# Performance work log

Hardware: AMD Instinct MI355X
Metric: run time of the kernel (lower is better)

The kernel has to match this reference:

```python
import jax, jax.numpy as jnp
import numpy as np

B, S, H, T, W = 8, 512, 768, 4, 10
NEG = -1e9

def _u(key, shape, k):
    return jax.random.uniform(key, shape, jnp.float32, -k, k)

def setup_inputs():
    key = jax.random.key(0)
    ks = jax.random.split(key, 20)
    kh = float(1.0 / np.sqrt(H)); kt = float(1.0 / np.sqrt(T))
    return dict(
        embeddings=jax.random.normal(ks[0], (B, S, H), jnp.float32),
        l1f_wih=_u(ks[1], (4 * H, H), kh), l1f_whh=_u(ks[2], (4 * H, H), kh), l1f_b=_u(ks[3], (4 * H,), kh),
        l1r_wih=_u(ks[4], (4 * H, H), kh), l1r_whh=_u(ks[5], (4 * H, H), kh), l1r_b=_u(ks[6], (4 * H,), kh),
        attn_w=_u(ks[7], (3 * H,), kh), attn_b=_u(ks[8], (1,), kh),
        l2f_wih=_u(ks[9], (4 * T, 2 * H), kt), l2f_whh=_u(ks[10], (4 * T, T), kt), l2f_b=_u(ks[11], (4 * T,), kt),
        l2r_wih=_u(ks[12], (4 * T, 2 * H), kt), l2r_whh=_u(ks[13], (4 * T, T), kt), l2r_b=_u(ks[14], (4 * T,), kt),
        crf_start=0.1 * jax.random.normal(ks[15], (T,), jnp.float32),
        crf_end=0.1 * jax.random.normal(ks[16], (T,), jnp.float32),
        crf_trans=0.1 * jax.random.normal(ks[17], (T, T), jnp.float32),
        window_size=W,
    )

def _lstm_dir(x, w_ih, w_hh, b):
    # x: [B,S,D] -> [B,S,Hh]; torch gate order i,f,g,o
    Hh = w_hh.shape[1]
    bs = x.shape[0]
    xs = (jnp.einsum('bsd,gd->bsg', x, w_ih) + b).transpose(1, 0, 2)  # [S,B,4Hh]
    def step(carry, xt):
        h, c = carry
        g = xt + h @ w_hh.T
        i, f, gg, o = jnp.split(g, 4, axis=-1)
        c = jax.nn.sigmoid(f) * c + jax.nn.sigmoid(i) * jnp.tanh(gg)
        h = jax.nn.sigmoid(o) * jnp.tanh(c)
        return (h, c), h
    init = (jnp.zeros((bs, Hh), x.dtype), jnp.zeros((bs, Hh), x.dtype))
    _, hs = jax.lax.scan(step, init, xs)
    return hs.transpose(1, 0, 2)

def _bilstm(x, pf, pr):
    hf = _lstm_dir(x, *pf)
    hr = _lstm_dir(x[:, ::-1], *pr)[:, ::-1]
    return jnp.concatenate([hf, hr], axis=-1)

def _win_attn(h, w, b, win):
    # h: [B,S,D]; similarity(hi,hj) = w1.hi + w2.hj + w3.(hi*hj) + b
    bs, s, d = h.shape
    w1, w2, w3 = w[:d], w[d:2 * d], w[2 * d:]
    offs = jnp.arange(-win, win + 1)                      # [K]
    idx = jnp.arange(s)[:, None] + offs[None, :]          # [S,K]
    valid = (idx >= 0) & (idx < s)
    idxc = jnp.clip(idx, 0, s - 1)
    hw = h[:, idxc]                                       # [B,S,K,D]
    scores = (h @ w1)[:, :, None] \
        + jnp.einsum('bskd,d->bsk', hw, w2) \
        + jnp.einsum('bsd,bskd->bsk', h * w3, hw) + b[0]
    scores = jnp.where(valid[None], scores, NEG)
    aw = jax.nn.softmax(scores, axis=-1)                  # [B,S,K]
    return jnp.einsum('bsk,bskd->bsd', aw, hw)

def _viterbi(em, start, end, trans):
    # em: [B,S,T] -> tags [B,S]
    score0 = start[None] + em[:, 0]
    ems = em.transpose(1, 0, 2)[1:]                       # [S-1,B,T]
    def step(score, e_t):
        nxt = score[:, :, None] + trans[None]             # [B,Tprev,T]
        best = jnp.max(nxt, axis=1) + e_t
        bp = jnp.argmax(nxt, axis=1)
        return best, bp
    final, bps = jax.lax.scan(step, score0, ems)          # bps [S-1,B,T]
    final = final + end[None]
    last = jnp.argmax(final, axis=-1)                     # [B]
    def back(tag, bp):
        prev = jnp.take_along_axis(bp, tag[:, None], axis=1)[:, 0]
        return prev, prev
    _, tags_rev = jax.lax.scan(back, last, bps[::-1])
    return jnp.concatenate([tags_rev[::-1], last[None]], axis=0).transpose(1, 0)

def reference(embeddings, l1f_wih, l1f_whh, l1f_b, l1r_wih, l1r_whh, l1r_b,
              attn_w, attn_b, l2f_wih, l2f_whh, l2f_b, l2r_wih, l2r_whh, l2r_b,
              crf_start, crf_end, crf_trans, window_size):
    h1 = _bilstm(embeddings, (l1f_wih, l1f_whh, l1f_b), (l1r_wih, l1r_whh, l1r_b))
    d = h1.shape[-1] // 2
    hs = h1[..., :d] + h1[..., d:]                        # sum of directions [B,S,H]
    att = _win_attn(hs, attn_w, attn_b, int(window_size))
    x2 = jnp.concatenate([hs, att], axis=-1)              # [B,S,2H]
    h2 = _bilstm(x2, (l2f_wih, l2f_whh, l2f_b), (l2r_wih, l2r_whh, l2r_b))
    d2 = h2.shape[-1] // 2
    em = h2[..., :d2] + h2[..., d2:]                      # CRF emissions [B,S,T]
    tags = _viterbi(em, crf_start, crf_end, crf_trans)
    return tags, em
```

## Files before the change

### kernel.cpp

```cpp
#include <hip/hip_runtime.h>
#include <math.h>

#define SEQ 512
#define BATCH 8
#define HID 768
#define G4 3072
#define CHUNK 128
#define NEGV (-1000000000.0f)

typedef float v4f __attribute__((ext_vector_type(4)));

__device__ __forceinline__ float sigm(float x) { return 1.0f / (1.0f + expf(-x)); }

__device__ __forceinline__ float wred(float x) {
#pragma unroll
  for (int off = 32; off > 0; off >>= 1) x += __shfl_xor(x, off, 64);
  return x;
}

__device__ __forceinline__ void load2_f4_sc(const float* p0, const float* p1,
                                            v4f& a, v4f& b) {
  asm volatile("global_load_dwordx4 %0, %2, off sc0 sc1\n\t"
               "global_load_dwordx4 %1, %3, off sc0 sc1\n\t"
               "s_waitcnt vmcnt(0)"
               : "=&v"(a), "=&v"(b) : "v"(p0), "v"(p1) : "memory");
}
__device__ __forceinline__ int load_i_sc(const int* p) {
  int r;
  asm volatile("global_load_dword %0, %1, off sc0 sc1\n\ts_waitcnt vmcnt(0)"
               : "=v"(r) : "v"(p) : "memory");
  return r;
}
__device__ __forceinline__ void store_f_sc(float* p, float v) {
  asm volatile("global_store_dword %0, %1, off sc0 sc1" :: "v"(p), "v"(v) : "memory");
}
__device__ __forceinline__ void store_i_sc(int* p, int v) {
  asm volatile("global_store_dword %0, %1, off sc0 sc1" :: "v"(p), "v"(v) : "memory");
}

template <int CTRL, int RMASK>
__device__ __forceinline__ float dpp_add(float x) {
  int y = __builtin_amdgcn_update_dpp(0, __float_as_int(x), CTRL, RMASK, 0xF, false);
  return x + __int_as_float(y);
}
__device__ __forceinline__ float reduce32(float x) {
  x = dpp_add<0x121, 0xF>(x);
  x = dpp_add<0x122, 0xF>(x);
  x = dpp_add<0x124, 0xF>(x);
  x = dpp_add<0x128, 0xF>(x);
  x = dpp_add<0x142, 0xA>(x);
  return x;
}

__global__ void k_init(float* __restrict__ hbuf, int* __restrict__ flags) {
  int i = blockIdx.x * blockDim.x + threadIdx.x;
  if (i < 2 * 2 * BATCH * HID) hbuf[i] = 0.0f;
  if (i < 4096) flags[i] = 0;
}

__global__ __launch_bounds__(256) void k_proj1(
    const float* __restrict__ emb,
    const float* __restrict__ w_f, const float* __restrict__ b_f,
    const float* __restrict__ w_r, const float* __restrict__ b_r,
    float* __restrict__ xs_f, float* __restrict__ xs_r, int chunk) {
  __shared__ float As[16][132];
  __shared__ float Bs[16][132];
  const int tid = threadIdx.x;
  const int bn0 = blockIdx.x * 128;
  const int bb  = blockIdx.y;
  const int dir = blockIdx.z;
  const float* W    = dir ? w_r : w_f;
  const float* bias = dir ? b_r : b_f;
  float* xs = dir ? xs_r : xs_f;

  float acc[8][8];
#pragma unroll
  for (int i = 0; i < 8; i++)
#pragma unroll
    for (int j = 0; j < 8; j++) acc[i][j] = 0.0f;

  const int mload = tid & 127;
  const int kq0   = tid >> 7;
  const int tglob = dir ? (SEQ - 1 - (chunk * CHUNK + mload)) : (chunk * CHUNK + mload);
  const float* arow = emb + (size_t)(bb * SEQ + tglob) * HID;
  const float* brow = W + (size_t)(bn0 + mload) * HID;
  const int tm = tid & 15, tn = tid >> 4;

  for (int kt = 0; kt < HID; kt += 16) {
#pragma unroll
    for (int rep = 0; rep < 2; rep++) {
      int kq = kq0 + rep * 2;
      float4 a = *(const float4*)(arow + kt + kq * 4);
      As[kq * 4 + 0][mload] = a.x; As[kq * 4 + 1][mload] = a.y;
      As[kq * 4 + 2][mload] = a.z; As[kq * 4 + 3][mload] = a.w;
      float4 b = *(const float4*)(brow + kt + kq * 4);
      Bs[kq * 4 + 0][mload] = b.x; Bs[kq * 4 + 1][mload] = b.y;
      Bs[kq * 4 + 2][mload] = b.z; Bs[kq * 4 + 3][mload] = b.w;
    }
    __syncthreads();
#pragma unroll
    for (int k = 0; k < 16; k++) {
      float4 a0 = *(const float4*)&As[k][tm * 8];
      float4 a1 = *(const float4*)&As[k][tm * 8 + 4];
      float4 b0 = *(const float4*)&Bs[k][tn * 8];
      float4 b1 = *(const float4*)&Bs[k][tn * 8 + 4];
      float av[8] = {a0.x, a0.y, a0.z, a0.w, a1.x, a1.y, a1.z, a1.w};
      float bv[8] = {b0.x, b0.y, b0.z, b0.w, b1.x, b1.y, b1.z, b1.w};
#pragma unroll
      for (int i = 0; i < 8; i++)
#pragma unroll
        for (int j = 0; j < 8; j++) acc[i][j] += av[i] * bv[j];
    }
    __syncthreads();
  }
#pragma unroll
  for (int i = 0; i < 8; i++) {
    int row = tm * 8 + i;
    size_t base = (size_t)(bb * CHUNK + row) * G4 + bn0 + tn * 8;
#pragma unroll
    for (int j = 0; j < 8; j++) xs[base + j] = acc[i][j] + bias[bn0 + tn * 8 + j];
  }
}

__global__ __launch_bounds__(384, 2) void k_rec1(
    const float* __restrict__ whh_f, const float* __restrict__ whh_r,
    const float* __restrict__ xs_f, const float* __restrict__ xs_r,
    float* __restrict__ hbuf, float* __restrict__ cbuf, int* __restrict__ flags,
    float* __restrict__ hf, float* __restrict__ hr, int t0, int init) {
  __shared__ float hlds[4 * HID];
  const int tid = threadIdx.x;
  const int bid = blockIdx.x;
  const int dir = bid >> 7;
  const int bh  = (bid >> 6) & 1;
  const int jb  = bid & 63;
  const int J0  = jb * 12;
  const int grp = dir * 2 + bh;
  const int g  = tid >> 5;
  const int kq = tid & 31;
  const int j  = J0 + g;

  const float* W  = dir ? whh_r : whh_f;
  const float* xs = dir ? xs_r  : xs_f;
  float* harr = dir ? hr : hf;

  float wreg[4][24];
#pragma unroll
  for (int gate = 0; gate < 4; gate++) {
#pragma unroll
    for (int q = 0; q < 6; q++) {
      *(v4f*)&wreg[gate][q * 4] =
          *(const v4f*)&W[(size_t)(gate * HID + j) * HID + q * 128 + kq * 4];
    }
  }

  float cc[4];
#pragma unroll
  for (int b = 0; b < 4; b++) cc[b] = 0.0f;
  if (!init && kq == 16) {
#pragma unroll
    for (int b = 0; b < 4; b++) cc[b] = cbuf[bid * 48 + g * 4 + b];
  }

  for (int stp = 0; stp < CHUNK; stp++) {
    const int s = t0 + stp;
    const int par = s & 1;

    float xsv[4][4];
    if (kq == 16) {
#pragma unroll
      for (int b = 0; b < 4; b++) {
        const size_t xbase = (size_t)((bh * 4 + b) * CHUNK + stp) * G4 + j;
#pragma unroll
        for (int gate = 0; gate < 4; gate++)
          xsv[b][gate] = xs[xbase + gate * HID];
      }
    }

    if (tid < 64) {
      const int* fp = flags + (grp * 64 + tid) * 16;
      while (load_i_sc(fp) < s) { __builtin_amdgcn_s_sleep(4); }
    }
    __syncthreads();

    {
      const float* src = hbuf + (size_t)((par * 2 + dir) * BATCH + bh * 4) * HID + tid * 8;
      v4f a, b4;
      load2_f4_sc(src, src + 4, a, b4);
      *(v4f*)&hlds[tid * 8]     = a;
      *(v4f*)&hlds[tid * 8 + 4] = b4;
    }
    __syncthreads();

    float acc[4][4];
#pragma unroll
    for (int gate = 0; gate < 4; gate++)
#pragma unroll
      for (int b = 0; b < 4; b++) acc[gate][b] = 0.0f;
#pragma unroll
    for (int b = 0; b < 4; b++) {
      float hk[24];
#pragma unroll
      for (int q = 0; q < 6; q++)
        *(v4f*)&hk[q * 4] = *(const v4f*)&hlds[b * HID + q * 128 + kq * 4];
#pragma unroll
      for (int gate = 0; gate < 4; gate++)
#pragma unroll
        for (int k = 0; k < 24; k++) acc[gate][b] += wreg[gate][k] * hk[k];
    }
#pragma unroll
    for (int gate = 0; gate < 4; gate++)
#pragma unroll
      for (int b = 0; b < 4; b++) acc[gate][b] = reduce32(acc[gate][b]);

    if (kq == 16) {
      const int t = dir ? (SEQ - 1 - s) : s;
#pragma unroll
      for (int b = 0; b < 4; b++) {
        const int bg = bh * 4 + b;
        float iv = acc[0][b] + xsv[b][0];
        float fv = acc[1][b] + xsv[b][1];
        float gv = acc[2][b] + xsv[b][2];
        float ov = acc[3][b] + xsv[b][3];
        cc[b] = sigm(fv) * cc[b] + sigm(iv) * tanhf(gv);
        float h = sigm(ov) * tanhf(cc[b]);
        store_f_sc(hbuf + (size_t)(((par ^ 1) * 2 + dir) * BATCH + bg) * HID + j, h);
        harr[(size_t)(bg * SEQ + t) * HID + j] = h;
      }
    }
    asm volatile("s_waitcnt vmcnt(0)" ::: "memory");
    __syncthreads();
    if (tid == 0) store_i_sc(flags + (grp * 64 + jb) * 16, s + 1);
  }
  if (kq == 16) {
#pragma unroll
    for (int b = 0; b < 4; b++) cbuf[bid * 48 + g * 4 + b] = cc[b];
  }
}

__global__ void k_sum(float* __restrict__ hf, const float* __restrict__ hr) {
  int i = blockIdx.x * 256 + threadIdx.x;
  float4 a = ((const float4*)hf)[i];
  float4 b = ((const float4*)hr)[i];
  a.x += b.x; a.y += b.y; a.z += b.z; a.w += b.w;
  ((float4*)hf)[i] = a;
}

__global__ __launch_bounds__(64) void k_attn(
    const float* __restrict__ hs, const float* __restrict__ attn_w,
    const float* __restrict__ attn_b, float* __restrict__ att) {
  const int l = threadIdx.x;
  const int s = blockIdx.x, b = blockIdx.y;
  const float* hrow = hs + (size_t)(b * SEQ + s) * HID;
  float v[12];
  float u1p = 0.0f;
#pragma unroll
  for (int jj = 0; jj < 12; jj++) {
    int d = l + 64 * jj;
    float x = hrow[d];
    u1p += x * attn_w[d];
    v[jj] = attn_w[HID + d] + x * attn_w[2 * HID + d];
  }
  float u1 = wred(u1p) + attn_b[0];
  float sc[21];
  for (int o = 0; o < 21; o++) {
    int s2 = s + o - 10;
    if (s2 >= 0 && s2 < SEQ) {
      const float* h2 = hs + (size_t)(b * SEQ + s2) * HID;
      float p = 0.0f;
#pragma unroll
      for (int jj = 0; jj < 12; jj++) p += h2[l + 64 * jj] * v[jj];
      sc[o] = wred(p) + u1;
    } else {
      sc[o] = NEGV;
    }
  }
  float m = sc[0];
#pragma unroll
  for (int o = 1; o < 21; o++) m = fmaxf(m, sc[o]);
  float sum = 0.0f;
#pragma unroll
  for (int o = 0; o < 21; o++) { sc[o] = expf(sc[o] - m); sum += sc[o]; }
  float inv = 1.0f / sum;
  float acc[12];
#pragma unroll
  for (int jj = 0; jj < 12; jj++) acc[jj] = 0.0f;
  for (int o = 0; o < 21; o++) {
    int s2 = s + o - 10;
    if (s2 < 0 || s2 >= SEQ) continue;
    float a = sc[o] * inv;
    const float* h2 = hs + (size_t)(b * SEQ + s2) * HID;
#pragma unroll
    for (int jj = 0; jj < 12; jj++) acc[jj] += a * h2[l + 64 * jj];
  }
  float* orow = att + (size_t)(b * SEQ + s) * HID;
#pragma unroll
  for (int jj = 0; jj < 12; jj++) orow[l + 64 * jj] = acc[jj];
}

__global__ __launch_bounds__(256) void k_proj2(
    const float* __restrict__ hs, const float* __restrict__ att,
    const float* __restrict__ w2f, const float* __restrict__ b2f,
    const float* __restrict__ w2r, const float* __restrict__ b2r,
    float* __restrict__ xs2) {
  __shared__ __align__(16) float x2[2 * HID];
  __shared__ float part[32][9];
  const int tid = threadIdx.x;
  const int s = blockIdx.x, b = blockIdx.y;
  size_t base = (size_t)(b * SEQ + s) * HID;
  for (int i = tid; i < 2 * HID; i += 256)
    x2[i] = (i < HID) ? hs[base + i] : att[base + i - HID];
  __syncthreads();
  const int gid = tid & 31, pp = tid >> 5;
  const int d = gid >> 4, g = gid & 15;
  const float4* w4 = (const float4*)((d ? w2r : w2f) + (size_t)g * (2 * HID));
  const float4* x4 = (const float4*)x2;
  float p = 0.0f;
  for (int e = pp * 48; e < pp * 48 + 48; e++) {
    float4 xv = x4[e];
    float4 wv = w4[e];
    p += xv.x * wv.x + xv.y * wv.y + xv.z * wv.z + xv.w * wv.w;
  }
  part[gid][pp] = p;
  __syncthreads();
  if (tid < 32) {
    float sumv = (d ? b2r : b2f)[g];
#pragma unroll
    for (int q = 0; q < 8; q++) sumv += part[gid][q];
    xs2[(size_t)((d * BATCH + b) * SEQ + s) * 16 + g] = sumv;
  }
}

__global__ __launch_bounds__(256) void k_rec2(
    const float* __restrict__ xs2,
    const float* __restrict__ whh_f, const float* __restrict__ whh_r,
    float* __restrict__ h2) {
  __shared__ float hsh[2 * BATCH * 4];
  __shared__ float gsh[2 * BATCH * 16];
  const int tid = threadIdx.x;
  const int d = tid >> 7, b = (tid >> 4) & 7, g = tid & 15;
  const float* whh = (d ? whh_r : whh_f) + g * 4;
  const float w0 = whh[0], w1 = whh[1], w2 = whh[2], w3 = whh[3];
  const int hb = d * BATCH + b;
  if (g < 4) hsh[hb * 4 + g] = 0.0f;
  float c = 0.0f;
  __syncthreads();
  const float* xrow = xs2 + (size_t)hb * SEQ * 16 + g;
  for (int st = 0; st < SEQ; st++) {
    int t = d ? (SEQ - 1 - st) : st;
    float gv = xrow[t * 16] + w0 * hsh[hb * 4 + 0] + w1 * hsh[hb * 4 + 1] +
               w2 * hsh[hb * 4 + 2] + w3 * hsh[hb * 4 + 3];
    gsh[hb * 16 + g] = gv;
    __syncthreads();
    if (g < 4) {
      float iv = gsh[hb * 16 + g];
      float fv = gsh[hb * 16 + 4 + g];
      float gq = gsh[hb * 16 + 8 + g];
      float ov = gsh[hb * 16 + 12 + g];
      c = sigm(fv) * c + sigm(iv) * tanhf(gq);
      float h = sigm(ov) * tanhf(c);
      hsh[hb * 4 + g] = h;
      h2[((size_t)hb * SEQ + t) * 4 + g] = h;
    }
    __syncthreads();
  }
}

__global__ void k_em(const float* __restrict__ h2, float* __restrict__ out) {
  int i = blockIdx.x * 256 + threadIdx.x;
  if (i < BATCH * SEQ * 4) out[BATCH * SEQ + i] = h2[i] + h2[BATCH * SEQ * 4 + i];
}

__global__ __launch_bounds__(32) void k_viterbi(
    float* __restrict__ out, const float* __restrict__ start,
    const float* __restrict__ endw, const float* __restrict__ trans) {
  __shared__ unsigned char bp[SEQ - 1][32];
  const int l = threadIdx.x;
  const int b = l >> 2, j = l & 3;
  const float* em = out + BATCH * SEQ;
  const float tr0 = trans[0 * 4 + j], tr1 = trans[1 * 4 + j];
  const float tr2 = trans[2 * 4 + j], tr3 = trans[3 * 4 + j];
  float score = start[j] + em[((size_t)b * SEQ + 0) * 4 + j];
  for (int t = 1; t < SEQ; t++) {
    float s0 = __shfl(score, b * 4 + 0, 64);
    float s1 = __shfl(score, b * 4 + 1, 64);
    float s2 = __shfl(score, b * 4 + 2, 64);
    float s3 = __shfl(score, b * 4 + 3, 64);
    float v0 = s0 + tr0, v1 = s1 + tr1, v2 = s2 + tr2, v3 = s3 + tr3;
    float best = v0; int arg = 0;
    if (v1 > best) { best = v1; arg = 1; }
    if (v2 > best) { best = v2; arg = 2; }
    if (v3 > best) { best = v3; arg = 3; }
    bp[t - 1][l] = (unsigned char)arg;
    score = best + em[((size_t)b * SEQ + t) * 4 + j];
  }
  score += endw[j];
  float f0 = __shfl(score, b * 4 + 0, 64);
  float f1 = __shfl(score, b * 4 + 1, 64);
  float f2 = __shfl(score, b * 4 + 2, 64);
  float f3 = __shfl(score, b * 4 + 3, 64);
  if (j == 0) {
    float bbv = f0; int last = 0;
    if (f1 > bbv) { bbv = f1; last = 1; }
    if (f2 > bbv) { bbv = f2; last = 2; }
    if (f3 > bbv) { bbv = f3; last = 3; }
    int tag = last;
    out[b * SEQ + (SEQ - 1)] = (float)tag;
    for (int t = SEQ - 2; t >= 0; t--) {
      tag = bp[t][b * 4 + tag];
      out[b * SEQ + t] = (float)tag;
    }
  }
}

extern "C" void kernel_launch(void* const* d_in, const int* in_sizes, int n_in,
                              void* d_out, int out_size, void* d_ws, size_t ws_size,
                              hipStream_t stream) {
  const float* emb      = (const float*)d_in[0];
  const float* l1f_wih  = (const float*)d_in[1];
  const float* l1f_whh  = (const float*)d_in[2];
  const float* l1f_b    = (const float*)d_in[3];
  const float* l1r_wih  = (const float*)d_in[4];
  const float* l1r_whh  = (const float*)d_in[5];
  const float* l1r_b    = (const float*)d_in[6];
  const float* attn_w   = (const float*)d_in[7];
  const float* attn_b   = (const float*)d_in[8];
  const float* l2f_wih  = (const float*)d_in[9];
  const float* l2f_whh  = (const float*)d_in[10];
  const float* l2f_b    = (const float*)d_in[11];
  const float* l2r_wih  = (const float*)d_in[12];
  const float* l2r_whh  = (const float*)d_in[13];
  const float* l2r_b    = (const float*)d_in[14];
  const float* crf_start= (const float*)d_in[15];
  const float* crf_end  = (const float*)d_in[16];
  const float* crf_trans= (const float*)d_in[17];

  float* ws = (float*)d_ws;
  const size_t NCH = (size_t)BATCH * CHUNK * G4;
  float* xs_f = ws;
  float* xs_r = xs_f + NCH;
  float* hf   = xs_r + NCH;
  float* hr   = hf + (size_t)BATCH * SEQ * HID;
  float* hbuf = hr + (size_t)BATCH * SEQ * HID;
  float* cbuf = hbuf + 2 * 2 * BATCH * HID;
  float* h2   = cbuf + 256 * 48;
  int*   flags= (int*)(h2 + 2 * BATCH * SEQ * 4);
  float* xs2  = xs_f;
  float* att  = xs_r;
  float* hs   = hf;

  k_init<<<dim3(96), dim3(256), 0, stream>>>(hbuf, flags);

  for (int c = 0; c < 4; c++) {
    k_proj1<<<dim3(24, 8, 2), dim3(256), 0, stream>>>(
        emb, l1f_wih, l1f_b, l1r_wih, l1r_b, xs_f, xs_r, c);
    k_rec1<<<dim3(256), dim3(384), 0, stream>>>(
        l1f_whh, l1r_whh, xs_f, xs_r, hbuf, cbuf, flags, hf, hr,
        c * CHUNK, c == 0 ? 1 : 0);
  }

  k_sum<<<dim3(3072), dim3(256), 0, stream>>>(hf, hr);
  k_attn<<<dim3(SEQ, BATCH), dim3(64), 0, stream>>>(hs, attn_w, attn_b, att);
  k_proj2<<<dim3(SEQ, BATCH), dim3(256), 0, stream>>>(
      hs, att, l2f_wih, l2f_b, l2r_wih, l2r_b, xs2);
  k_rec2<<<dim3(1), dim3(256), 0, stream>>>(xs2, l2f_whh, l2r_whh, h2);
  k_em<<<dim3(64), dim3(256), 0, stream>>>(h2, (float*)d_out);
  k_viterbi<<<dim3(1), dim3(32), 0, stream>>>((float*)d_out, crf_start, crf_end, crf_trans);
}
```

Measured before the change: 3.860 ms.

## Use packed FMA in projection and recurrence, shuffle-based layer-2 LSTM

Switches the layer-1 projection GEMM and the recurrent matvec to two-wide vector FMA, so the compiler can emit packed FP32 FMA instructions. In the recurrence, gate weights are interleaved into pairs for this. It also shortens the sleep in the cross-block flag spin-wait to cut polling latency. The small layer-2 LSTM is rewritten to exchange h and gate values through wave shuffles instead of LDS and two __syncthreads per step, and it prefetches the next input. Risks are changed register pressure in k_rec1 under launch_bounds(384,2) and more contention on the flag polls.

```diff
diff --git a/kernel.cpp b/kernel.cpp
--- a/kernel.cpp
+++ b/kernel.cpp
@@ -9,8 +9,18 @@
 #define NEGV (-1000000000.0f)
 
 typedef float v4f __attribute__((ext_vector_type(4)));
+typedef float v2f __attribute__((ext_vector_type(2)));
 
 __device__ __forceinline__ float sigm(float x) { return 1.0f / (1.0f + expf(-x)); }
+
+__device__ __forceinline__ v2f fma2(v2f a, v2f b, v2f c) {
+#if __has_builtin(__builtin_elementwise_fma)
+  return __builtin_elementwise_fma(a, b, c);
+#else
+  v2f r; r.x = __builtin_fmaf(a.x, b.x, c.x); r.y = __builtin_fmaf(a.y, b.y, c.y);
+  return r;
+#endif
+}
 
 __device__ __forceinline__ float wred(float x) {
 #pragma unroll
@@ -73,11 +83,11 @@
   const float* bias = dir ? b_r : b_f;
   float* xs = dir ? xs_r : xs_f;
 
-  float acc[8][8];
+  v2f acc2[8][4];
 #pragma unroll
   for (int i = 0; i < 8; i++)
 #pragma unroll
-    for (int j = 0; j < 8; j++) acc[i][j] = 0.0f;
+    for (int j = 0; j < 4; j++) acc2[i][j] = (v2f){0.0f, 0.0f};
 
   const int mload = tid & 127;
   const int kq0   = tid >> 7;
@@ -105,11 +115,13 @@
       float4 b0 = *(const float4*)&Bs[k][tn * 8];
       float4 b1 = *(const float4*)&Bs[k][tn * 8 + 4];
       float av[8] = {a0.x, a0.y, a0.z, a0.w, a1.x, a1.y, a1.z, a1.w};
-      float bv[8] = {b0.x, b0.y, b0.z, b0.w, b1.x, b1.y, b1.z, b1.w};
-#pragma unroll
-      for (int i = 0; i < 8; i++)
-#pragma unroll
-        for (int j = 0; j < 8; j++) acc[i][j] += av[i] * bv[j];
+      v2f bv2[4] = {{b0.x, b0.y}, {b0.z, b0.w}, {b1.x, b1.y}, {b1.z, b1.w}};
+#pragma unroll
+      for (int i = 0; i < 8; i++) {
+        v2f avv = {av[i], av[i]};
+#pragma unroll
+        for (int jj = 0; jj < 4; jj++) acc2[i][jj] = fma2(avv, bv2[jj], acc2[i][jj]);
+      }
     }
     __syncthreads();
   }
@@ -118,7 +130,10 @@
     int row = tm * 8 + i;
     size_t base = (size_t)(bb * CHUNK + row) * G4 + bn0 + tn * 8;
 #pragma unroll
-    for (int j = 0; j < 8; j++) xs[base + j] = acc[i][j] + bias[bn0 + tn * 8 + j];
+    for (int jj = 0; jj < 4; jj++) {
+      xs[base + 2 * jj]     = acc2[i][jj].x + bias[bn0 + tn * 8 + 2 * jj];
+      xs[base + 2 * jj + 1] = acc2[i][jj].y + bias[bn0 + tn * 8 + 2 * jj + 1];
+    }
   }
 }
 
@@ -143,13 +158,17 @@
   const float* xs = dir ? xs_r  : xs_f;
   float* harr = dir ? hr : hf;
 
-  float wreg[4][24];
+  v2f wreg2[2][24];
 #pragma unroll
   for (int gate = 0; gate < 4; gate++) {
 #pragma unroll
     for (int q = 0; q < 6; q++) {
-      *(v4f*)&wreg[gate][q * 4] =
-          *(const v4f*)&W[(size_t)(gate * HID + j) * HID + q * 128 + kq * 4];
+      v4f w = *(const v4f*)&W[(size_t)(gate * HID + j) * HID + q * 128 + kq * 4];
+#pragma unroll
+      for (int e = 0; e < 4; e++) {
+        if (gate & 1) wreg2[gate >> 1][q * 4 + e].y = w[e];
+        else          wreg2[gate >> 1][q * 4 + e].x = w[e];
+      }
     }
   }
 
@@ -178,7 +197,7 @@
 
     if (tid < 64) {
       const int* fp = flags + (grp * 64 + tid) * 16;
-      while (load_i_sc(fp) < s) { __builtin_amdgcn_s_sleep(4); }
+      while (load_i_sc(fp) < s) { __builtin_amdgcn_s_sleep(1); }
     }
     __syncthreads();
 
@@ -191,11 +210,11 @@
     }
     __syncthreads();
 
-    float acc[4][4];
-#pragma unroll
-    for (int gate = 0; gate < 4; gate++)
-#pragma unroll
-      for (int b = 0; b < 4; b++) acc[gate][b] = 0.0f;
+    v2f acc2[2][4];
+#pragma unroll
+    for (int gp = 0; gp < 2; gp++)
+#pragma unroll
+      for (int b = 0; b < 4; b++) acc2[gp][b] = (v2f){0.0f, 0.0f};
 #pragma unroll
     for (int b = 0; b < 4; b++) {
       float hk[24];
@@ -203,24 +222,30 @@
       for (int q = 0; q < 6; q++)
         *(v4f*)&hk[q * 4] = *(const v4f*)&hlds[b * HID + q * 128 + kq * 4];
 #pragma unroll
-      for (int gate = 0; gate < 4; gate++)
-#pragma unroll
-        for (int k = 0; k < 24; k++) acc[gate][b] += wreg[gate][k] * hk[k];
-    }
-#pragma unroll
-    for (int gate = 0; gate < 4; gate++)
-#pragma unroll
-      for (int b = 0; b < 4; b++) acc[gate][b] = reduce32(acc[gate][b]);
+      for (int k = 0; k < 24; k++) {
+        v2f hv = {hk[k], hk[k]};
+        acc2[0][b] = fma2(wreg2[0][k], hv, acc2[0][b]);
+        acc2[1][b] = fma2(wreg2[1][k], hv, acc2[1][b]);
+      }
+    }
+    float accs[4][4];
+#pragma unroll
+    for (int gp = 0; gp < 2; gp++)
+#pragma unroll
+      for (int b = 0; b < 4; b++) {
+        accs[2 * gp][b]     = reduce32(acc2[gp][b].x);
+        accs[2 * gp + 1][b] = reduce32(acc2[gp][b].y);
+      }
 
     if (kq == 16) {
       const int t = dir ? (SEQ - 1 - s) : s;
 #pragma unroll
       for (int b = 0; b < 4; b++) {
         const int bg = bh * 4 + b;
-        float iv = acc[0][b] + xsv[b][0];
-        float fv = acc[1][b] + xsv[b][1];
-        float gv = acc[2][b] + xsv[b][2];
-        float ov = acc[3][b] + xsv[b][3];
+        float iv = accs[0][b] + xsv[b][0];
+        float fv = accs[1][b] + xsv[b][1];
+        float gv = accs[2][b] + xsv[b][2];
+        float ov = accs[3][b] + xsv[b][3];
         cc[b] = sigm(fv) * cc[b] + sigm(iv) * tanhf(gv);
         float h = sigm(ov) * tanhf(cc[b]);
         store_f_sc(hbuf + (size_t)(((par ^ 1) * 2 + dir) * BATCH + bg) * HID + j, h);
@@ -334,34 +359,35 @@
     const float* __restrict__ xs2,
     const float* __restrict__ whh_f, const float* __restrict__ whh_r,
     float* __restrict__ h2) {
-  __shared__ float hsh[2 * BATCH * 4];
-  __shared__ float gsh[2 * BATCH * 16];
   const int tid = threadIdx.x;
-  const int d = tid >> 7, b = (tid >> 4) & 7, g = tid & 15;
+  const int lane = tid & 63;
+  const int hb = (tid >> 6) * 4 + (lane >> 4);
+  const int g = lane & 15;
+  const int d = hb >> 3;
+  const int base = lane & 48;
   const float* whh = (d ? whh_r : whh_f) + g * 4;
   const float w0 = whh[0], w1 = whh[1], w2 = whh[2], w3 = whh[3];
-  const int hb = d * BATCH + b;
-  if (g < 4) hsh[hb * 4 + g] = 0.0f;
-  float c = 0.0f;
-  __syncthreads();
   const float* xrow = xs2 + (size_t)hb * SEQ * 16 + g;
+  float c = 0.0f, h = 0.0f;
+  float xv = xrow[(d ? (SEQ - 1) : 0) * 16];
   for (int st = 0; st < SEQ; st++) {
-    int t = d ? (SEQ - 1 - st) : st;
-    float gv = xrow[t * 16] + w0 * hsh[hb * 4 + 0] + w1 * hsh[hb * 4 + 1] +
-               w2 * hsh[hb * 4 + 2] + w3 * hsh[hb * 4 + 3];
-    gsh[hb * 16 + g] = gv;
-    __syncthreads();
-    if (g < 4) {
-      float iv = gsh[hb * 16 + g];
-      float fv = gsh[hb * 16 + 4 + g];
-      float gq = gsh[hb * 16 + 8 + g];
-      float ov = gsh[hb * 16 + 12 + g];
-      c = sigm(fv) * c + sigm(iv) * tanhf(gq);
-      float h = sigm(ov) * tanhf(c);
-      hsh[hb * 4 + g] = h;
-      h2[((size_t)hb * SEQ + t) * 4 + g] = h;
-    }
-    __syncthreads();
+    const int t = d ? (SEQ - 1 - st) : st;
+    const int tn = d ? (SEQ - 2 - st) : (st + 1);
+    float xnext = (st + 1 < SEQ) ? xrow[tn * 16] : 0.0f;
+    float h0 = __shfl(h, base + 0, 64);
+    float h1 = __shfl(h, base + 1, 64);
+    float h2v = __shfl(h, base + 2, 64);
+    float h3 = __shfl(h, base + 3, 64);
+    float gv = xv + w0 * h0 + w1 * h1 + w2 * h2v + w3 * h3;
+    const int jj = g & 3;
+    float iv = __shfl(gv, base + jj, 64);
+    float fv = __shfl(gv, base + 4 + jj, 64);
+    float gq = __shfl(gv, base + 8 + jj, 64);
+    float ov = __shfl(gv, base + 12 + jj, 64);
+    c = sigm(fv) * c + sigm(iv) * tanhf(gq);
+    h = sigm(ov) * tanhf(c);
+    if (g < 4) h2[((size_t)hb * SEQ + t) * 4 + g] = h;
+    xv = xnext;
   }
 }
 
```

New measurement: 3.846 ms. Within noise of the previous version (-0.3%).
